# Kernel tuning notes

Measured on AMD Instinct MI355X. Metric: run time of the kernel, lower is better.

## Reference

```python
import jax, jax.numpy as jnp
import numpy as np

N, E, F_IN = 100000, 1000000, 128
H, C = 4, 32
HC = H * C
D_DIR = 128
G = 250
HID, CLS = 128, 2
ALPHA = 0.5
NEG = 0.2  # LeakyReLU slope in GATv2


def setup_inputs() -> dict:
    key = jax.random.key(0)
    ks = jax.random.split(key, 16)
    p = lambda k, shape: 0.02 * jax.random.normal(k, shape, jnp.float32)
    return {
        "x": jax.random.normal(ks[0], (N, F_IN), jnp.float32),
        "edge_index": jax.random.randint(ks[1], (2, E), 0, N, dtype=jnp.int32),
        "edge_attr": jax.random.normal(ks[2], (E, 1), jnp.float32),
        "batch": jnp.sort(jax.random.randint(ks[3], (N,), 0, G, dtype=jnp.int32)),
        "dir_w_in": p(ks[4], (2, F_IN, D_DIR)),
        "dir_b_in": jnp.zeros((2, D_DIR), jnp.float32),
        "dir_w_out": p(ks[5], (2, F_IN, D_DIR)),
        "dir_b_out": jnp.zeros((2, D_DIR), jnp.float32),
        "gat_wl": p(ks[6], (F_IN, HC)),
        "gat_wr": p(ks[7], (F_IN, HC)),
        "gat_we": p(ks[8], (1, HC)),
        "gat_att": p(ks[9], (H, C)),
        "gat_b": jnp.zeros((HC,), jnp.float32),
        "w1": p(ks[10], (D_DIR + HC, HID)),
        "b1": jnp.zeros((HID,), jnp.float32),
        "w2": p(ks[11], (HID, CLS)),
        "b2": jnp.zeros((CLS,), jnp.float32),
    }


def _gcn(x, src, dst, W, b):
    # GCNConv with add_self_loops=False (forced by DirGNNConv), unit edge weights.
    deg = jnp.zeros((N,), x.dtype).at[dst].add(1.0)
    dinv = jnp.where(deg > 0, 1.0 / jnp.sqrt(jnp.maximum(deg, 1.0)), 0.0)
    norm = dinv[src] * dinv[dst]  # [E]
    h = x @ W  # [N, D]
    out = jnp.zeros((N, W.shape[1]), x.dtype).at[dst].add(norm[:, None] * h[src])
    return out + b


def _mean_pool(h, batch):
    cnt = jnp.zeros((G,), h.dtype).at[batch].add(1.0)
    s = jnp.zeros((G, h.shape[1]), h.dtype).at[batch].add(h)
    return s / jnp.maximum(cnt, 1.0)[:, None]


def _forward(x, edge_index, edge_attr, batch, dir_w_in, dir_b_in, dir_w_out, dir_b_out,
             gat_wl, gat_wr, gat_we, gat_att, gat_b, w1, b1, w2, b2):
    src, dst = edge_index[0], edge_index[1]
    # --- DirGNN branch: alpha * GCN(flipped edges) + (1-alpha) * GCN(edges), relu between ---
    h = x
    for i in range(2):
        x_in = _gcn(h, src, dst, dir_w_in[i], dir_b_in[i])
        x_out = _gcn(h, dst, src, dir_w_out[i], dir_b_out[i])
        h = jax.nn.relu(ALPHA * x_out + (1.0 - ALPHA) * x_in)
    x1 = _mean_pool(h, batch)  # [G, D_DIR]
    # --- GATv2 branch (self loops appended, edge_attr fill value 1.0) ---
    loop = jnp.arange(N, dtype=src.dtype)
    s2 = jnp.concatenate([src, loop])
    d2 = jnp.concatenate([dst, loop])
    ea = jnp.concatenate([edge_attr, jnp.ones((N, 1), edge_attr.dtype)], axis=0)
    gl = (x @ gat_wl).reshape(N, H, C)  # source transform
    gr = (x @ gat_wr).reshape(N, H, C)  # target transform
    ee = (ea @ gat_we).reshape(-1, H, C)
    e = jax.nn.leaky_relu(gl[s2] + gr[d2] + ee, NEG)  # [E+N, H, C]
    logits = jnp.einsum('ehc,hc->eh', e, gat_att)
    # segment softmax over incoming edges of each target node (self loops => nonempty)
    m = jnp.full((N, H), -jnp.inf, logits.dtype).at[d2].max(logits)
    ex = jnp.exp(logits - m[d2])
    denom = jnp.zeros((N, H), logits.dtype).at[d2].add(ex)
    att = ex / denom[d2]
    out2 = jnp.zeros((N, H, C), x.dtype).at[d2].add(att[:, :, None] * gl[s2])
    x2 = _mean_pool(out2.reshape(N, HC) + gat_b, batch)  # [G, HC]
    # --- head ---
    z = jnp.concatenate([x1, x2], axis=1)
    z = jax.nn.relu(z @ w1 + b1)
    return z @ w2 + b2  # [G, CLS]


def reference(x, edge_index, edge_attr, batch, dir_w_in, dir_b_in, dir_w_out, dir_b_out,
              gat_wl, gat_wr, gat_we, gat_att, gat_b, w1, b1, w2, b2):
    return _forward(x, edge_index, edge_attr, batch, dir_w_in, dir_b_in, dir_w_out, dir_b_out,
                    gat_wl, gat_wr, gat_we, gat_att, gat_b, w1, b1, w2, b2)
```

## Files before the change

### kernel.cpp

```cpp
#include <hip/hip_runtime.h>
#include <cstdint>

#define FDIM 128
#define PCH 64

static inline int cdiv(long long a, long long b) { return (int)((a + b - 1) / b); }

__global__ __launch_bounds__(256) void degi_kernel(const int* __restrict__ src,
                                                   const int* __restrict__ dst,
                                                   int* __restrict__ deg_in,
                                                   int* __restrict__ deg_out, int E) {
  int base = (blockIdx.x * 256 + threadIdx.x) * 2;
  if (base + 2 <= E) {
    int2 s2 = *(const int2*)(src + base);
    int2 d2 = *(const int2*)(dst + base);
    atomicAdd(&deg_in[d2.x], 1);
    atomicAdd(&deg_in[d2.y], 1);
    atomicAdd(&deg_out[s2.x], 1);
    atomicAdd(&deg_out[s2.y], 1);
  } else {
    for (int i = base; i < E; i++) {
      atomicAdd(&deg_in[dst[i]], 1);
      atomicAdd(&deg_out[src[i]], 1);
    }
  }
}

__global__ __launch_bounds__(256) void dinv2_kernel(const int* __restrict__ degs,
                                                    float* __restrict__ dinv, int n2) {
  int i = blockIdx.x * 256 + threadIdx.x;
  if (i < n2) {
    int v = degs[i];
    dinv[i] = v > 0 ? 1.0f / sqrtf((float)v) : 0.f;
  }
}

__global__ __launch_bounds__(256) void cnt_sorted(const int* __restrict__ batch,
                                                  float* __restrict__ cnt, int N, int G) {
  int g = blockIdx.x * 256 + threadIdx.x;
  if (g >= G) return;
  int lo = 0, hi = N;
  while (lo < hi) { int mid = (lo + hi) >> 1; if (batch[mid] < g) lo = mid + 1; else hi = mid; }
  int lo2 = lo, hi2 = N;
  while (lo2 < hi2) { int mid = (lo2 + hi2) >> 1; if (batch[mid] <= g) lo2 = mid + 1; else hi2 = mid; }
  cnt[g] = (float)(lo2 - lo);
}

__global__ __launch_bounds__(256) void scan1(const int* __restrict__ in, int* __restrict__ out,
                                             int* __restrict__ bsums, int n) {
  __shared__ int tmp[256];
  int t = threadIdx.x;
  int base = blockIdx.x * 1024 + t * 4;
  int a[4];
#pragma unroll
  for (int j = 0; j < 4; j++) a[j] = (base + j < n) ? in[base + j] : 0;
  int s = a[0] + a[1] + a[2] + a[3];
  tmp[t] = s;
  __syncthreads();
  for (int off = 1; off < 256; off <<= 1) {
    int v = (t >= off) ? tmp[t - off] : 0;
    __syncthreads();
    tmp[t] += v;
    __syncthreads();
  }
  int excl = tmp[t] - s;
  int run = excl;
#pragma unroll
  for (int j = 0; j < 4; j++) {
    if (base + j < n) out[base + j] = run;
    run += a[j];
  }
  if (t == 255) bsums[blockIdx.x] = tmp[255];
}

__global__ __launch_bounds__(256) void scan2(const int* __restrict__ bsums,
                                             int* __restrict__ boff, int nb) {
  __shared__ int tmp[256];
  int t = threadIdx.x;
  int s = (t < nb) ? bsums[t] : 0;
  tmp[t] = s;
  __syncthreads();
  for (int off = 1; off < 256; off <<= 1) {
    int v = (t >= off) ? tmp[t - off] : 0;
    __syncthreads();
    tmp[t] += v;
    __syncthreads();
  }
  if (t < nb) boff[t] = tmp[t] - s;
}

__global__ __launch_bounds__(256) void scan3(const int* __restrict__ scanned,
                                             const int* __restrict__ boff,
                                             int* __restrict__ rp_in, int* __restrict__ cur_in,
                                             int* __restrict__ rp_out, int* __restrict__ cur_out,
                                             int N, int E, int n2) {
  int i = blockIdx.x * 256 + threadIdx.x;
  if (i < n2) {
    int v = scanned[i] + boff[i >> 10];
    if (i < N) { rp_in[i] = v; cur_in[i] = v; }
    else { v -= E; rp_out[i - N] = v; cur_out[i - N] = v; }
  }
}

__global__ __launch_bounds__(256) void fill_kernel(const int* __restrict__ src,
                                                   const int* __restrict__ dst,
                                                   const float* __restrict__ eattr,
                                                   int* __restrict__ cur_in,
                                                   int* __restrict__ cur_out,
                                                   int2* __restrict__ csr_in,
                                                   int* __restrict__ csr_out_dst, int E) {
  int base = (blockIdx.x * 256 + threadIdx.x) * 2;
  if (base + 2 <= E) {
    int2 s2 = *(const int2*)(src + base);
    int2 d2 = *(const int2*)(dst + base);
    float2 e2 = *(const float2*)(eattr + base);
    int p0 = atomicAdd(&cur_in[d2.x], 1);
    int p1 = atomicAdd(&cur_in[d2.y], 1);
    int q0 = atomicAdd(&cur_out[s2.x], 1);
    int q1 = atomicAdd(&cur_out[s2.y], 1);
    csr_in[p0] = make_int2(s2.x, __float_as_int(e2.x));
    csr_in[p1] = make_int2(s2.y, __float_as_int(e2.y));
    csr_out_dst[q0] = d2.x;
    csr_out_dst[q1] = d2.y;
  } else {
    for (int i = base; i < E; i++) {
      int s = src[i], d = dst[i];
      int p = atomicAdd(&cur_in[d], 1);
      csr_in[p] = make_int2(s, __float_as_int(eattr[i]));
      int q = atomicAdd(&cur_out[s], 1);
      csr_out_dst[q] = d;
    }
  }
}

__global__ __launch_bounds__(256) void mm128d(const float* __restrict__ A,
                                              const float* __restrict__ W0,
                                              const float* __restrict__ W1,
                                              float* __restrict__ out0,
                                              float* __restrict__ out1, int nrows) {
  __shared__ float As[64][128];
  __shared__ float Ws[64][64];
  int r0 = blockIdx.x * 64;
  int tid = threadIdx.x;

#pragma unroll
  for (int i = 0; i < 8; i++) {
    int v = tid + 256 * i;
    int r = v >> 5, k4 = (v & 31) << 2;
    int row = r0 + r;
    float4 a;
    if (row < nrows) a = *(const float4*)(A + (size_t)row * FDIM + k4);
    else a = make_float4(0.f, 0.f, 0.f, 0.f);
    int swz = ((r >> 2) & 7) << 2;
    *(float4*)(&As[r][k4 ^ swz]) = a;
  }

  int tx = tid & 15, ty = tid >> 4;
  int rbase = ty * 4;
  int swz = (ty & 7) << 2;

  for (int p = 0; p < 4; p++) {
    const float* W = (p < 2) ? W0 : W1;
    float* out = (p < 2) ? out0 : out1;
    int cb = (p & 1) * 64;
    float acc[4][4] = {};

    for (int kh = 0; kh < 2; kh++) {
      __syncthreads();
#pragma unroll
      for (int i = 0; i < 4; i++) {
        int v = tid + 256 * i;
        int k = v >> 4, c4 = (v & 15) << 2;
        *(float4*)(&Ws[k][c4]) = *(const float4*)(W + (kh * 64 + k) * FDIM + cb + c4);
      }
      __syncthreads();

#pragma unroll 8
      for (int k = 0; k < 64; k++) {
        int kx = (kh * 64 + k) ^ swz;
        float a0 = As[rbase + 0][kx];
        float a1 = As[rbase + 1][kx];
        float a2 = As[rbase + 2][kx];
        float a3 = As[rbase + 3][kx];
        float4 w = *(float4*)(&Ws[k][tx * 4]);
        acc[0][0] += a0 * w.x; acc[0][1] += a0 * w.y; acc[0][2] += a0 * w.z; acc[0][3] += a0 * w.w;
        acc[1][0] += a1 * w.x; acc[1][1] += a1 * w.y; acc[1][2] += a1 * w.z; acc[1][3] += a1 * w.w;
        acc[2][0] += a2 * w.x; acc[2][1] += a2 * w.y; acc[2][2] += a2 * w.z; acc[2][3] += a2 * w.w;
        acc[3][0] += a3 * w.x; acc[3][1] += a3 * w.y; acc[3][2] += a3 * w.z; acc[3][3] += a3 * w.w;
      }
    }

#pragma unroll
    for (int rr = 0; rr < 4; rr++) {
      int row = r0 + rbase + rr;
      if (row < nrows) {
        float4 o = make_float4(acc[rr][0], acc[rr][1], acc[rr][2], acc[rr][3]);
        *(float4*)(out + (size_t)row * FDIM + cb + tx * 4) = o;
      }
    }
  }
}

__global__ __launch_bounds__(128) void gcn_gather4(const float4* __restrict__ tin,
                                                   const float4* __restrict__ tout,
                                                   const int* __restrict__ rp_in,
                                                   const int* __restrict__ deg_in,
                                                   const int2* __restrict__ adj_in,
                                                   const int* __restrict__ rp_out,
                                                   const int* __restrict__ deg_out,
                                                   const int* __restrict__ adj_out,
                                                   const float* __restrict__ dinv_in,
                                                   const float* __restrict__ dinv_out,
                                                   const float* __restrict__ bin,
                                                   const float* __restrict__ bout,
                                                   float4* __restrict__ outp, int N) {
  int grp = threadIdx.x >> 5, lane = threadIdx.x & 31;
  int d = blockIdx.x * 4 + grp;
  if (d >= N) return;
  float wi = 0.5f * dinv_in[d], wo = 0.5f * dinv_out[d];
  float4 a0 = make_float4(0.f, 0.f, 0.f, 0.f);
  float4 a1 = a0, a2 = a0, a3 = a0;

  int p = rp_in[d], n1 = deg_in[d];
  int k = 0;
  for (; k + 4 <= n1; k += 4) {
    int s0 = adj_in[p + k].x, s1 = adj_in[p + k + 1].x, s2 = adj_in[p + k + 2].x, s3 = adj_in[p + k + 3].x;
    float w0 = wi * dinv_in[s0], w1 = wi * dinv_in[s1], w2 = wi * dinv_in[s2], w3 = wi * dinv_in[s3];
    float4 v0 = tin[(size_t)s0 * 32 + lane];
    float4 v1 = tin[(size_t)s1 * 32 + lane];
    float4 v2 = tin[(size_t)s2 * 32 + lane];
    float4 v3 = tin[(size_t)s3 * 32 + lane];
    a0.x += w0 * v0.x; a0.y += w0 * v0.y; a0.z += w0 * v0.z; a0.w += w0 * v0.w;
    a1.x += w1 * v1.x; a1.y += w1 * v1.y; a1.z += w1 * v1.z; a1.w += w1 * v1.w;
    a2.x += w2 * v2.x; a2.y += w2 * v2.y; a2.z += w2 * v2.z; a2.w += w2 * v2.w;
    a3.x += w3 * v3.x; a3.y += w3 * v3.y; a3.z += w3 * v3.z; a3.w += w3 * v3.w;
  }
  for (; k < n1; k++) {
    int s = adj_in[p + k].x;
    float w = wi * dinv_in[s];
    float4 v = tin[(size_t)s * 32 + lane];
    a0.x += w * v.x; a0.y += w * v.y; a0.z += w * v.z; a0.w += w * v.w;
  }

  int q = rp_out[d], n2 = deg_out[d];
  k = 0;
  for (; k + 4 <= n2; k += 4) {
    int s0 = adj_out[q + k], s1 = adj_out[q + k + 1], s2 = adj_out[q + k + 2], s3 = adj_out[q + k + 3];
    float w0 = wo * dinv_out[s0], w1 = wo * dinv_out[s1], w2 = wo * dinv_out[s2], w3 = wo * dinv_out[s3];
    float4 v0 = tout[(size_t)s0 * 32 + lane];
    float4 v1 = tout[(size_t)s1 * 32 + lane];
    float4 v2 = tout[(size_t)s2 * 32 + lane];
    float4 v3 = tout[(size_t)s3 * 32 + lane];
    a0.x += w0 * v0.x; a0.y += w0 * v0.y; a0.z += w0 * v0.z; a0.w += w0 * v0.w;
    a1.x += w1 * v1.x; a1.y += w1 * v1.y; a1.z += w1 * v1.z; a1.w += w1 * v1.w;
    a2.x += w2 * v2.x; a2.y += w2 * v2.y; a2.z += w2 * v2.z; a2.w += w2 * v2.w;
    a3.x += w3 * v3.x; a3.y += w3 * v3.y; a3.z += w3 * v3.z; a3.w += w3 * v3.w;
  }
  for (; k < n2; k++) {
    int s = adj_out[q + k];
    float w = wo * dinv_out[s];
    float4 v = tout[(size_t)s * 32 + lane];
    a0.x += w * v.x; a0.y += w * v.y; a0.z += w * v.z; a0.w += w * v.w;
  }

  float4 acc;
  acc.x = (a0.x + a1.x) + (a2.x + a3.x);
  acc.y = (a0.y + a1.y) + (a2.y + a3.y);
  acc.z = (a0.z + a1.z) + (a2.z + a3.z);
  acc.w = (a0.w + a1.w) + (a2.w + a3.w);

  const float4* b1 = (const float4*)bin;
  const float4* b2 = (const float4*)bout;
  float4 ba = b1[lane], bb = b2[lane];
  float4 o;
  o.x = acc.x + 0.5f * (ba.x + bb.x);
  o.y = acc.y + 0.5f * (ba.y + bb.y);
  o.z = acc.z + 0.5f * (ba.z + bb.z);
  o.w = acc.w + 0.5f * (ba.w + bb.w);
  o.x = o.x > 0.f ? o.x : 0.f;
  o.y = o.y > 0.f ? o.y : 0.f;
  o.z = o.z > 0.f ? o.z : 0.f;
  o.w = o.w > 0.f ? o.w : 0.f;
  outp[(size_t)d * 32 + lane] = o;
}

__global__ __launch_bounds__(128) void gat_fused2(const float4* __restrict__ gl,
                                                  const float4* __restrict__ gr,
                                                  const int* __restrict__ rp,
                                                  const int* __restrict__ deg,
                                                  const int2* __restrict__ adj,
                                                  const float* __restrict__ we,
                                                  const float* __restrict__ att,
                                                  const float* __restrict__ gatb,
                                                  float4* __restrict__ outp, int N) {
  int grp = threadIdx.x >> 5, lane = threadIdx.x & 31;
  int d = blockIdx.x * 4 + grp;
  if (d >= N) return;

  float4 grv = gr[(size_t)d * 32 + lane];
  float4 wev = ((const float4*)we)[lane];
  float4 atv = ((const float4*)att)[lane];

  int p = rp[d], n1 = deg[d];
  float m = -1e30f, den = 0.f;
  float4 o = make_float4(0.f, 0.f, 0.f, 0.f);

#define GAT_LOGIT(g4, ea, pv)                                                     \
  {                                                                               \
    float vx = g4.x + grv.x + (ea) * wev.x; vx = vx > 0.f ? vx : 0.2f * vx;       \
    float vy = g4.y + grv.y + (ea) * wev.y; vy = vy > 0.f ? vy : 0.2f * vy;       \
    float vz = g4.z + grv.z + (ea) * wev.z; vz = vz > 0.f ? vz : 0.2f * vz;       \
    float vw = g4.w + grv.w + (ea) * wev.w; vw = vw > 0.f ? vw : 0.2f * vw;       \
    pv = vx * atv.x + vy * atv.y + vz * atv.z + vw * atv.w;                       \
    pv += __shfl_xor(pv, 1);                                                      \
    pv += __shfl_xor(pv, 2);                                                      \
    pv += __shfl_xor(pv, 4);                                                      \
  }

#define GAT_UPDATE(g4, pv)                                                        \
  {                                                                               \
    float mn = fmaxf(m, pv);                                                      \
    float sc = expf(m - mn);                                                      \
    float w = expf(pv - mn);                                                      \
    den = den * sc + w;                                                           \
    o.x = o.x * sc + w * g4.x;                                                    \
    o.y = o.y * sc + w * g4.y;                                                    \
    o.z = o.z * sc + w * g4.z;                                                    \
    o.w = o.w * sc + w * g4.w;                                                    \
    m = mn;                                                                       \
  }

  int k = 0;
  for (; k + 2 <= n1; k += 2) {
    int2 e0 = adj[p + k], e1 = adj[p + k + 1];
    int s0 = e0.x, s1 = e1.x;
    float ea0 = __int_as_float(e0.y), ea1 = __int_as_float(e1.y);
    float4 g0 = gl[(size_t)s0 * 32 + lane];
    float4 g1 = gl[(size_t)s1 * 32 + lane];
    float pv0, pv1;
    GAT_LOGIT(g0, ea0, pv0);
    GAT_LOGIT(g1, ea1, pv1);
    GAT_UPDATE(g0, pv0);
    GAT_UPDATE(g1, pv1);
  }
  if (k < n1) {
    int2 e = adj[p + k];
    float ea = __int_as_float(e.y);
    float4 g = gl[(size_t)e.x * 32 + lane];
    float pv;
    GAT_LOGIT(g, ea, pv);
    GAT_UPDATE(g, pv);
  }
  {
    float4 g = gl[(size_t)d * 32 + lane];
    float pv;
    GAT_LOGIT(g, 1.0f, pv);
    GAT_UPDATE(g, pv);
  }
#undef GAT_LOGIT
#undef GAT_UPDATE

  float4 bb = ((const float4*)gatb)[lane];
  float4 r;
  r.x = o.x / den + bb.x;
  r.y = o.y / den + bb.y;
  r.z = o.z / den + bb.z;
  r.w = o.w / den + bb.w;
  outp[(size_t)d * 32 + lane] = r;
}

__global__ __launch_bounds__(128) void pool_kernel(const float* __restrict__ srcf,
                                                   const int* __restrict__ batch,
                                                   float* __restrict__ zb,
                                                   int colOff, int N) {
  __shared__ int sb[PCH];
  int c0 = blockIdx.x * PCH;
  int t = threadIdx.x;
  int nmax = N - c0; if (nmax > PCH) nmax = PCH;
  if (t < nmax) sb[t] = batch[c0 + t];
  __syncthreads();
  float run = 0.f;
  int gp = sb[0];
  for (int i = 0; i < nmax; i++) {
    int g = sb[i];
    if (g != gp) {
      atomicAdd(&zb[(size_t)gp * 256 + colOff + t], run);
      run = 0.f; gp = g;
    }
    run += srcf[(size_t)(c0 + i) * FDIM + t];
  }
  atomicAdd(&zb[(size_t)gp * 256 + colOff + t], run);
}

__global__ __launch_bounds__(128) void head_kernel(const float* __restrict__ zb,
                                                   const float* __restrict__ cnt,
                                                   const float* __restrict__ w1,
                                                   const float* __restrict__ b1,
                                                   const float* __restrict__ w2,
                                                   const float* __restrict__ b2,
                                                   float* __restrict__ out, int G) {
  __shared__ float z[256];
  __shared__ float y[128];
  int g = blockIdx.x, t = threadIdx.x;
  float c = cnt[g];
  float cm = c > 1.f ? c : 1.f;
  z[t]       = zb[(size_t)g * 256 + t] / cm;
  z[t + 128] = zb[(size_t)g * 256 + 128 + t] / cm;
  __syncthreads();
  float acc = b1[t];
  for (int k = 0; k < 256; k++) acc += z[k] * w1[k * 128 + t];
  y[t] = acc > 0.f ? acc : 0.f;
  __syncthreads();
  if (t < 2) {
    float o = b2[t];
    for (int j = 0; j < 128; j++) o += y[j] * w2[j * 2 + t];
    out[(size_t)g * 2 + t] = o;
  }
}

extern "C" void kernel_launch(void* const* d_in, const int* in_sizes, int n_in,
                              void* d_out, int out_size, void* d_ws, size_t ws_size,
                              hipStream_t stream) {
  const float* x     = (const float*)d_in[0];
  const int*   ei    = (const int*)d_in[1];
  const float* eattr = (const float*)d_in[2];
  const int*   batch = (const int*)d_in[3];
  const float* dwi   = (const float*)d_in[4];
  const float* dbi   = (const float*)d_in[5];
  const float* dwo   = (const float*)d_in[6];
  const float* dbo   = (const float*)d_in[7];
  const float* wl    = (const float*)d_in[8];
  const float* wr    = (const float*)d_in[9];
  const float* we    = (const float*)d_in[10];
  const float* att   = (const float*)d_in[11];
  const float* gatb  = (const float*)d_in[12];
  const float* w1    = (const float*)d_in[13];
  const float* b1    = (const float*)d_in[14];
  const float* w2    = (const float*)d_in[15];
  const float* b2    = (const float*)d_in[16];

  int N = in_sizes[0] / FDIM;
  int E = in_sizes[1] / 2;
  int G = out_size / 2;
  const int* src = ei;
  const int* dst = ei + E;

  float* ws = (float*)d_ws;
  size_t off = 0;
  float* A        = ws + off; off += (size_t)N * FDIM;
  float* B        = ws + off; off += (size_t)N * FDIM;
  float* C        = ws + off; off += (size_t)N * FDIM;
  float* dinv2    = ws + off; off += 2 * (size_t)N;
  int* deg2       = (int*)(ws + off); off += 2 * (size_t)N;
  int* rpt        = (int*)(ws + off); off += 2 * (size_t)N;
  int* rp_in      = (int*)(ws + off); off += (size_t)N;
  int* rp_out     = (int*)(ws + off); off += (size_t)N;
  int* cur_in     = (int*)(ws + off); off += (size_t)N;
  int* cur_out    = (int*)(ws + off); off += (size_t)N;
  int2* csr_in    = (int2*)(ws + off); off += 2 * (size_t)E;
  int* csr_out_dst= (int*)(ws + off); off += (size_t)E;
  int* bsums      = (int*)(ws + off); off += 256;
  int* boff       = (int*)(ws + off); off += 256;
  float* zb       = ws + off; off += (size_t)G * 256;
  float* cnt      = ws + off; off += (size_t)G;

  int* deg_in = deg2, *deg_out = deg2 + N;
  float* dinv_in = dinv2, *dinv_out = dinv2 + N;

  int n2 = 2 * N;
  int nb1 = cdiv(n2, 1024);

  hipMemsetAsync(deg2, 0, (size_t)n2 * sizeof(int), stream);
  degi_kernel<<<cdiv(E, 512), 256, 0, stream>>>(src, dst, deg_in, deg_out, E);
  dinv2_kernel<<<cdiv((long long)n2, 256), 256, 0, stream>>>(deg2, dinv2, n2);
  scan1<<<nb1, 256, 0, stream>>>(deg2, rpt, bsums, n2);
  scan2<<<1, 256, 0, stream>>>(bsums, boff, nb1);
  scan3<<<cdiv(n2, 256), 256, 0, stream>>>(rpt, boff, rp_in, cur_in, rp_out, cur_out, N, E, n2);
  fill_kernel<<<cdiv(E, 512), 256, 0, stream>>>(src, dst, eattr, cur_in, cur_out,
                                                csr_in, csr_out_dst, E);

  hipMemsetAsync(zb, 0, (size_t)G * 256 * sizeof(float), stream);
  cnt_sorted<<<cdiv(G, 256), 256, 0, stream>>>(batch, cnt, N, G);

  mm128d<<<cdiv(N, 64), 256, 0, stream>>>(x, dwi, dwo, B, C, N);
  gcn_gather4<<<cdiv(N, 4), 128, 0, stream>>>((const float4*)B, (const float4*)C,
                                              rp_in, deg_in, csr_in,
                                              rp_out, deg_out, csr_out_dst,
                                              dinv_in, dinv_out, dbi, dbo, (float4*)A, N);
  mm128d<<<cdiv(N, 64), 256, 0, stream>>>(A, dwi + 16384, dwo + 16384, B, C, N);
  gcn_gather4<<<cdiv(N, 4), 128, 0, stream>>>((const float4*)B, (const float4*)C,
                                              rp_in, deg_in, csr_in,
                                              rp_out, deg_out, csr_out_dst,
                                              dinv_in, dinv_out, dbi + 128, dbo + 128, (float4*)A, N);
  pool_kernel<<<cdiv(N, PCH), 128, 0, stream>>>(A, batch, zb, 0, N);

  mm128d<<<cdiv(N, 64), 256, 0, stream>>>(x, wl, wr, B, C, N);
  gat_fused2<<<cdiv(N, 4), 128, 0, stream>>>((const float4*)B, (const float4*)C,
                                             rp_in, deg_in, csr_in,
                                             we, att, gatb, (float4*)A, N);
  pool_kernel<<<cdiv(N, PCH), 128, 0, stream>>>(A, batch, zb, 128, N);

  head_kernel<<<G, 128, 0, stream>>>(zb, cnt, w1, b1, w2, b2, (float*)d_out, G);
}
```

Baseline: 1.183 ms.

## Fuse CSR fill into first matmul launch via interleaved block roles

```diff
diff --git a/kernel.cpp b/kernel.cpp
--- a/kernel.cpp
+++ b/kernel.cpp
@@ -102,33 +102,117 @@
   }
 }
 
-__global__ __launch_bounds__(256) void fill_kernel(const int* __restrict__ src,
-                                                   const int* __restrict__ dst,
-                                                   const float* __restrict__ eattr,
-                                                   int* __restrict__ cur_in,
-                                                   int* __restrict__ cur_out,
-                                                   int2* __restrict__ csr_in,
-                                                   int* __restrict__ csr_out_dst, int E) {
-  int base = (blockIdx.x * 256 + threadIdx.x) * 2;
-  if (base + 2 <= E) {
-    int2 s2 = *(const int2*)(src + base);
-    int2 d2 = *(const int2*)(dst + base);
-    float2 e2 = *(const float2*)(eattr + base);
-    int p0 = atomicAdd(&cur_in[d2.x], 1);
-    int p1 = atomicAdd(&cur_in[d2.y], 1);
-    int q0 = atomicAdd(&cur_out[s2.x], 1);
-    int q1 = atomicAdd(&cur_out[s2.y], 1);
-    csr_in[p0] = make_int2(s2.x, __float_as_int(e2.x));
-    csr_in[p1] = make_int2(s2.y, __float_as_int(e2.y));
-    csr_out_dst[q0] = d2.x;
-    csr_out_dst[q1] = d2.y;
-  } else {
-    for (int i = base; i < E; i++) {
-      int s = src[i], d = dst[i];
-      int p = atomicAdd(&cur_in[d], 1);
-      csr_in[p] = make_int2(s, __float_as_int(eattr[i]));
-      int q = atomicAdd(&cur_out[s], 1);
-      csr_out_dst[q] = d;
+__global__ __launch_bounds__(256) void mm0_fill(const float* __restrict__ A,
+                                                const float* __restrict__ W0,
+                                                const float* __restrict__ W1,
+                                                float* __restrict__ out0,
+                                                float* __restrict__ out1, int nrows, int mmB,
+                                                const int* __restrict__ src,
+                                                const int* __restrict__ dst,
+                                                const float* __restrict__ eattr,
+                                                int* __restrict__ cur_in,
+                                                int* __restrict__ cur_out,
+                                                int2* __restrict__ csr_in,
+                                                int* __restrict__ csr_out_dst, int E, int fillB) {
+  __shared__ float As[64][128];
+  __shared__ float Ws[64][64];
+  int T = mmB + fillB;
+  int bid = blockIdx.x;
+  int tid = threadIdx.x;
+  long long f0 = (long long)bid * fillB / T;
+  long long f1 = (long long)(bid + 1) * fillB / T;
+
+  if (f1 > f0) {
+    int base = ((int)f0 * 256 + tid) * 4;
+    if (base + 4 <= E) {
+      int4 s4 = *(const int4*)(src + base);
+      int4 d4 = *(const int4*)(dst + base);
+      float4 e4 = *(const float4*)(eattr + base);
+      int p0 = atomicAdd(&cur_in[d4.x], 1);
+      int p1 = atomicAdd(&cur_in[d4.y], 1);
+      int p2 = atomicAdd(&cur_in[d4.z], 1);
+      int p3 = atomicAdd(&cur_in[d4.w], 1);
+      int q0 = atomicAdd(&cur_out[s4.x], 1);
+      int q1 = atomicAdd(&cur_out[s4.y], 1);
+      int q2 = atomicAdd(&cur_out[s4.z], 1);
+      int q3 = atomicAdd(&cur_out[s4.w], 1);
+      csr_in[p0] = make_int2(s4.x, __float_as_int(e4.x));
+      csr_in[p1] = make_int2(s4.y, __float_as_int(e4.y));
+      csr_in[p2] = make_int2(s4.z, __float_as_int(e4.z));
+      csr_in[p3] = make_int2(s4.w, __float_as_int(e4.w));
+      csr_out_dst[q0] = d4.x;
+      csr_out_dst[q1] = d4.y;
+      csr_out_dst[q2] = d4.z;
+      csr_out_dst[q3] = d4.w;
+    } else {
+      for (int i = base; i < E; i++) {
+        int s = src[i], d = dst[i];
+        int p = atomicAdd(&cur_in[d], 1);
+        csr_in[p] = make_int2(s, __float_as_int(eattr[i]));
+        int q = atomicAdd(&cur_out[s], 1);
+        csr_out_dst[q] = d;
+      }
+    }
+    return;
+  }
+
+  int mb = bid - (int)f0;
+  int r0 = mb * 64;
+
+#pragma unroll
+  for (int i = 0; i < 8; i++) {
+    int v = tid + 256 * i;
+    int r = v >> 5, k4 = (v & 31) << 2;
+    int row = r0 + r;
+    float4 a;
+    if (row < nrows) a = *(const float4*)(A + (size_t)row * FDIM + k4);
+    else a = make_float4(0.f, 0.f, 0.f, 0.f);
+    int swz = ((r >> 2) & 7) << 2;
+    *(float4*)(&As[r][k4 ^ swz]) = a;
+  }
+
+  int tx = tid & 15, ty = tid >> 4;
+  int rbase = ty * 4;
+  int swz = (ty & 7) << 2;
+
+  for (int p = 0; p < 4; p++) {
+    const float* W = (p < 2) ? W0 : W1;
+    float* out = (p < 2) ? out0 : out1;
+    int cb = (p & 1) * 64;
+    float acc[4][4] = {};
+
+    for (int kh = 0; kh < 2; kh++) {
+      __syncthreads();
+#pragma unroll
+      for (int i = 0; i < 4; i++) {
+        int v = tid + 256 * i;
+        int k = v >> 4, c4 = (v & 15) << 2;
+        *(float4*)(&Ws[k][c4]) = *(const float4*)(W + (kh * 64 + k) * FDIM + cb + c4);
+      }
+      __syncthreads();
+
+#pragma unroll 8
+      for (int k = 0; k < 64; k++) {
+        int kx = (kh * 64 + k) ^ swz;
+        float a0 = As[rbase + 0][kx];
+        float a1 = As[rbase + 1][kx];
+        float a2 = As[rbase + 2][kx];
+        float a3 = As[rbase + 3][kx];
+        float4 w = *(float4*)(&Ws[k][tx * 4]);
+        acc[0][0] += a0 * w.x; acc[0][1] += a0 * w.y; acc[0][2] += a0 * w.z; acc[0][3] += a0 * w.w;
+        acc[1][0] += a1 * w.x; acc[1][1] += a1 * w.y; acc[1][2] += a1 * w.z; acc[1][3] += a1 * w.w;
+        acc[2][0] += a2 * w.x; acc[2][1] += a2 * w.y; acc[2][2] += a2 * w.z; acc[2][3] += a2 * w.w;
+        acc[3][0] += a3 * w.x; acc[3][1] += a3 * w.y; acc[3][2] += a3 * w.z; acc[3][3] += a3 * w.w;
+      }
+    }
+
+#pragma unroll
+    for (int rr = 0; rr < 4; rr++) {
+      int row = r0 + rbase + rr;
+      if (row < nrows) {
+        float4 o = make_float4(acc[rr][0], acc[rr][1], acc[rr][2], acc[rr][3]);
+        *(float4*)(out + (size_t)row * FDIM + cb + tx * 4) = o;
+      }
     }
   }
 }
@@ -476,25 +560,28 @@
   scan1<<<nb1, 256, 0, stream>>>(deg2, rpt, bsums, n2);
   scan2<<<1, 256, 0, stream>>>(bsums, boff, nb1);
   scan3<<<cdiv(n2, 256), 256, 0, stream>>>(rpt, boff, rp_in, cur_in, rp_out, cur_out, N, E, n2);
-  fill_kernel<<<cdiv(E, 512), 256, 0, stream>>>(src, dst, eattr, cur_in, cur_out,
-                                                csr_in, csr_out_dst, E);
 
   hipMemsetAsync(zb, 0, (size_t)G * 256 * sizeof(float), stream);
   cnt_sorted<<<cdiv(G, 256), 256, 0, stream>>>(batch, cnt, N, G);
 
-  mm128d<<<cdiv(N, 64), 256, 0, stream>>>(x, dwi, dwo, B, C, N);
+  int mmB = cdiv(N, 64);
+  int fillB = cdiv(E, 1024);
+  mm0_fill<<<mmB + fillB, 256, 0, stream>>>(x, dwi, dwo, B, C, N, mmB,
+                                            src, dst, eattr, cur_in, cur_out,
+                                            csr_in, csr_out_dst, E, fillB);
+
   gcn_gather4<<<cdiv(N, 4), 128, 0, stream>>>((const float4*)B, (const float4*)C,
                                               rp_in, deg_in, csr_in,
                                               rp_out, deg_out, csr_out_dst,
                                               dinv_in, dinv_out, dbi, dbo, (float4*)A, N);
-  mm128d<<<cdiv(N, 64), 256, 0, stream>>>(A, dwi + 16384, dwo + 16384, B, C, N);
+  mm128d<<<mmB, 256, 0, stream>>>(A, dwi + 16384, dwo + 16384, B, C, N);
   gcn_gather4<<<cdiv(N, 4), 128, 0, stream>>>((const float4*)B, (const float4*)C,
                                               rp_in, deg_in, csr_in,
                                               rp_out, deg_out, csr_out_dst,
                                               dinv_in, dinv_out, dbi + 128, dbo + 128, (float4*)A, N);
   pool_kernel<<<cdiv(N, PCH), 128, 0, stream>>>(A, batch, zb, 0, N);
 
-  mm128d<<<cdiv(N, 64), 256, 0, stream>>>(x, wl, wr, B, C, N);
+  mm128d<<<mmB, 256, 0, stream>>>(x, wl, wr, B, C, N);
   gat_fused2<<<cdiv(N, 4), 128, 0, stream>>>((const float4*)B, (const float4*)C,
                                              rp_in, deg_in, csr_in,
                                              we, att, gatb, (float4*)A, N);
```

Measured after the change: 1.082 ms. -8.5%, faster.
